# Kernel tuning notes

Hardware: AMD Instinct MI355X
Metric: run time of the kernel (lower is better)

The kernel has to match this reference:

```python
import jax, jax.numpy as jnp
import numpy as np

N_NODES = 100000
HIDDEN = 128
N_EDGES = 640000


def setup_inputs() -> dict:
    key = jax.random.key(0)
    ks = jax.random.split(key, 7)
    x = jax.random.normal(ks[0], (N_NODES, HIDDEN), dtype=jnp.float32)
    # torch Linear weights, stored transposed for y = h @ W + b
    W1 = jax.random.normal(ks[1], (HIDDEN, HIDDEN), dtype=jnp.float32) * (1.0 / np.sqrt(HIDDEN))
    b1 = jax.random.normal(ks[2], (HIDDEN,), dtype=jnp.float32) * 0.01
    W2 = jax.random.normal(ks[3], (HIDDEN, 1), dtype=jnp.float32) * (1.0 / np.sqrt(HIDDEN))
    b2 = jax.random.normal(ks[4], (1,), dtype=jnp.float32) * 0.01
    edge_index = jax.random.randint(ks[5], (2, N_EDGES), 0, N_NODES, dtype=jnp.int64 if jax.config.jax_enable_x64 else jnp.int32)
    edge_index_neg = jax.random.randint(ks[6], (2, N_EDGES), 0, N_NODES, dtype=jnp.int64 if jax.config.jax_enable_x64 else jnp.int32)
    return {"x": x, "W1": W1, "b1": b1, "W2": W2, "b2": b2,
            "edge_index": edge_index, "edge_index_neg": edge_index_neg}


def _decode(x, W1, b1, W2, b2, ei):
    # gather endpoints and Hadamard product: [E, hidden]
    h = x[ei[0]] * x[ei[1]]
    # decoder = ReLU -> Linear(h,h) -> ReLU -> Linear(h,1); then sigmoid
    h = jax.nn.relu(h)
    h = jax.nn.relu(h @ W1 + b1)
    return jax.nn.sigmoid(h @ W2 + b2)  # [E, 1]


def reference(x, W1, b1, W2, b2, edge_index, edge_index_neg):
    edge_pos_pred = _decode(x, W1, b1, W2, b2, edge_index)
    edge_neg_pred = _decode(x, W1, b1, W2, b2, edge_index_neg)
    return jnp.concatenate([edge_pos_pred, edge_neg_pred], axis=0)  # [2E, 1]
```

## Files before the change

### kernel.cpp

```cpp
#include <hip/hip_runtime.h>
#include <hip/hip_bf16.h>

#define HID   128
#define PITCH 136
#define TPB   256

typedef __attribute__((ext_vector_type(8))) __bf16 bf16x8;
typedef __attribute__((ext_vector_type(4))) __bf16 bf16x4;
typedef __attribute__((ext_vector_type(4))) float  f32x4;

__global__ __launch_bounds__(TPB) void prep_kernel(
    const float* __restrict__ W1, __bf16* __restrict__ w1t,
    const float* __restrict__ x, __bf16* __restrict__ xb, int n_x4) {
  if (xb) {
    for (int i = blockIdx.x * TPB + threadIdx.x; i < n_x4; i += gridDim.x * TPB) {
      float4 a = reinterpret_cast<const float4*>(x)[i];
      bf16x4 v;
      v[0] = (__bf16)a.x; v[1] = (__bf16)a.y; v[2] = (__bf16)a.z; v[3] = (__bf16)a.w;
      reinterpret_cast<bf16x4*>(xb)[i] = v;
    }
  }
  if (blockIdx.x == 0 && w1t) {
    __shared__ float w[HID * HID];
    for (int i = threadIdx.x; i < HID * HID; i += TPB) w[i] = W1[i];
    __syncthreads();
    for (int c = threadIdx.x; c < HID * (HID / 8); c += TPB) {
      int n  = c >> 4;
      int k0 = (c & 15) << 3;
      bf16x8 v;
#pragma unroll
      for (int j = 0; j < 8; ++j) v[j] = (__bf16)w[(k0 + j) * HID + n];
      *reinterpret_cast<bf16x8*>(&w1t[n * PITCH + k0]) = v;
    }
  }
}

__global__ __launch_bounds__(TPB) void vgae_decode_kernel(
    const __bf16* __restrict__ xb,
    const __bf16* __restrict__ w1t,
    const float* __restrict__ b1,
    const float* __restrict__ W2,
    const float* __restrict__ b2,
    const int* __restrict__ eip,
    const int* __restrict__ ein,
    float* __restrict__ out,
    int E, int n_tiles)
{
  __shared__ __bf16 sW[HID * PITCH];
  __shared__ float  sb1[HID];
  __shared__ float  sw2[HID];

  {
    const uint4* srcp = reinterpret_cast<const uint4*>(w1t);
    uint4*       dstp = reinterpret_cast<uint4*>(sW);
    for (int i = threadIdx.x; i < (HID * PITCH) / 8; i += TPB) dstp[i] = srcp[i];
  }
  if (threadIdx.x < HID) {
    sb1[threadIdx.x] = b1[threadIdx.x];
    sw2[threadIdx.x] = W2[threadIdx.x];
  }
  __syncthreads();

  const int lane = threadIdx.x & 63;
  const int wave = threadIdx.x >> 6;
  const int m    = lane & 15;
  const int quad = lane >> 4;
  const float b2v = b2[0];

  int tile = blockIdx.x;
  int nsrc = 0, ndst = 0;
  if (tile < n_tiles) {
    const int e_base = tile * 64 + wave * 16;
    const int* ei = (e_base < E) ? eip : ein;
    const int  eo = (e_base < E) ? e_base : (e_base - E);
    nsrc = ei[eo + m];
    ndst = ei[E + eo + m];
  }

  for (; tile < n_tiles; tile += gridDim.x) {
    const int src = nsrc, dst = ndst;
    const __bf16* xs = xb + (size_t)src * HID;
    const __bf16* xd = xb + (size_t)dst * HID;

    bf16x8 S[4], D[4];
#pragma unroll
    for (int kt = 0; kt < 4; ++kt) {
      const int k0 = kt * 32 + quad * 8;
      S[kt] = *reinterpret_cast<const bf16x8*>(xs + k0);
      D[kt] = *reinterpret_cast<const bf16x8*>(xd + k0);
    }

    const int tn = tile + gridDim.x;
    if (tn < n_tiles) {
      const int e_base = tn * 64 + wave * 16;
      const int* ei = (e_base < E) ? eip : ein;
      const int  eo = (e_base < E) ? e_base : (e_base - E);
      nsrc = ei[eo + m];
      ndst = ei[E + eo + m];
    }

    f32x4 acc[8] = {};

#pragma unroll
    for (int kt = 0; kt < 4; ++kt) {
      const int k0 = kt * 32 + quad * 8;
      bf16x8 a;
#pragma unroll
      for (int j = 0; j < 8; ++j) {
        float p = (float)S[kt][j] * (float)D[kt][j];
        a[j] = (__bf16)fmaxf(p, 0.f);
      }
#pragma unroll
      for (int nt = 0; nt < 8; ++nt) {
        bf16x8 bfr = *reinterpret_cast<const bf16x8*>(&sW[(nt * 16 + m) * PITCH + k0]);
        acc[nt] = __builtin_amdgcn_mfma_f32_16x16x32_bf16(a, bfr, acc[nt], 0, 0, 0);
      }
    }

    float p[4] = {0.f, 0.f, 0.f, 0.f};
#pragma unroll
    for (int nt = 0; nt < 8; ++nt) {
      const int n = nt * 16 + m;
      const float b1n = sb1[n];
      const float w2n = sw2[n];
#pragma unroll
      for (int r = 0; r < 4; ++r) {
        float t = fmaxf(acc[nt][r] + b1n, 0.f);
        p[r] = fmaf(t, w2n, p[r]);
      }
    }
#pragma unroll
    for (int off = 1; off < 16; off <<= 1) {
#pragma unroll
      for (int r = 0; r < 4; ++r) p[r] += __shfl_xor(p[r], off, 64);
    }
    if (m == 0) {
      float4 o;
      o.x = 1.f / (1.f + __expf(-(p[0] + b2v)));
      o.y = 1.f / (1.f + __expf(-(p[1] + b2v)));
      o.z = 1.f / (1.f + __expf(-(p[2] + b2v)));
      o.w = 1.f / (1.f + __expf(-(p[3] + b2v)));
      *reinterpret_cast<float4*>(out + tile * 64 + wave * 16 + quad * 4) = o;
    }
  }
}

__global__ __launch_bounds__(TPB) void vgae_decode_fallback(
    const float* __restrict__ x,
    const float* __restrict__ W1,
    const float* __restrict__ b1,
    const float* __restrict__ W2,
    const float* __restrict__ b2,
    const int* __restrict__ eip,
    const int* __restrict__ ein,
    float* __restrict__ out,
    int E, int n_tiles)
{
  __shared__ __bf16 sW[HID * PITCH];
  __shared__ float  sb1[HID];
  __shared__ float  sw2[HID];
  for (int c = threadIdx.x; c < HID * (HID / 8); c += TPB) {
    int n = c >> 4, k0 = (c & 15) << 3;
    bf16x8 v;
#pragma unroll
    for (int j = 0; j < 8; ++j) v[j] = (__bf16)W1[(k0 + j) * HID + n];
    *reinterpret_cast<bf16x8*>(&sW[n * PITCH + k0]) = v;
  }
  if (threadIdx.x < HID) { sb1[threadIdx.x] = b1[threadIdx.x]; sw2[threadIdx.x] = W2[threadIdx.x]; }
  __syncthreads();
  const int lane = threadIdx.x & 63, wave = threadIdx.x >> 6;
  const int m = lane & 15, quad = lane >> 4;
  const float b2v = b2[0];
  for (int tile = blockIdx.x; tile < n_tiles; tile += gridDim.x) {
    const int e_base = tile * 64 + wave * 16;
    const int* ei = (e_base < E) ? eip : ein;
    const int  eo = (e_base < E) ? e_base : (e_base - E);
    const int src = ei[eo + m], dst = ei[E + eo + m];
    const float* xs = x + (size_t)src * HID;
    const float* xd = x + (size_t)dst * HID;
    f32x4 acc[8] = {};
#pragma unroll
    for (int kt = 0; kt < 4; ++kt) {
      const int k0 = kt * 32 + quad * 8;
      float4 s0 = *reinterpret_cast<const float4*>(xs + k0);
      float4 s1 = *reinterpret_cast<const float4*>(xs + k0 + 4);
      float4 d0 = *reinterpret_cast<const float4*>(xd + k0);
      float4 d1 = *reinterpret_cast<const float4*>(xd + k0 + 4);
      bf16x8 a;
      a[0] = (__bf16)fmaxf(s0.x * d0.x, 0.f); a[1] = (__bf16)fmaxf(s0.y * d0.y, 0.f);
      a[2] = (__bf16)fmaxf(s0.z * d0.z, 0.f); a[3] = (__bf16)fmaxf(s0.w * d0.w, 0.f);
      a[4] = (__bf16)fmaxf(s1.x * d1.x, 0.f); a[5] = (__bf16)fmaxf(s1.y * d1.y, 0.f);
      a[6] = (__bf16)fmaxf(s1.z * d1.z, 0.f); a[7] = (__bf16)fmaxf(s1.w * d1.w, 0.f);
#pragma unroll
      for (int nt = 0; nt < 8; ++nt) {
        bf16x8 bfr = *reinterpret_cast<const bf16x8*>(&sW[(nt * 16 + m) * PITCH + k0]);
        acc[nt] = __builtin_amdgcn_mfma_f32_16x16x32_bf16(a, bfr, acc[nt], 0, 0, 0);
      }
    }
    float p[4] = {0.f, 0.f, 0.f, 0.f};
#pragma unroll
    for (int nt = 0; nt < 8; ++nt) {
      const int n = nt * 16 + m;
      const float b1n = sb1[n], w2n = sw2[n];
#pragma unroll
      for (int r = 0; r < 4; ++r) p[r] = fmaf(fmaxf(acc[nt][r] + b1n, 0.f), w2n, p[r]);
    }
#pragma unroll
    for (int off = 1; off < 16; off <<= 1)
#pragma unroll
      for (int r = 0; r < 4; ++r) p[r] += __shfl_xor(p[r], off, 64);
    if (m == 0) {
      float4 o;
      o.x = 1.f / (1.f + __expf(-(p[0] + b2v)));
      o.y = 1.f / (1.f + __expf(-(p[1] + b2v)));
      o.z = 1.f / (1.f + __expf(-(p[2] + b2v)));
      o.w = 1.f / (1.f + __expf(-(p[3] + b2v)));
      *reinterpret_cast<float4*>(out + tile * 64 + wave * 16 + quad * 4) = o;
    }
  }
}

extern "C" void kernel_launch(void* const* d_in, const int* in_sizes, int n_in,
                              void* d_out, int out_size, void* d_ws, size_t ws_size,
                              hipStream_t stream) {
  const float* x  = (const float*)d_in[0];
  const float* W1 = (const float*)d_in[1];
  const float* b1 = (const float*)d_in[2];
  const float* W2 = (const float*)d_in[3];
  const float* b2 = (const float*)d_in[4];
  const int*  eip = (const int*)d_in[5];
  const int*  ein = (const int*)d_in[6];
  float* out = (float*)d_out;
  const int E = in_sizes[5] / 2;
  const int n_tiles = (2 * E) / 64;
  const int n_nodes = in_sizes[0] / HID;
  const int n_x4 = in_sizes[0] / 4;

  const size_t w1t_bytes = (size_t)HID * PITCH * sizeof(__bf16);
  const size_t xb_off    = 65536;
  const size_t xb_bytes  = (size_t)n_nodes * HID * sizeof(__bf16);

  __bf16* w1t = nullptr;
  __bf16* xb  = nullptr;
  if (ws_size >= w1t_bytes) w1t = (__bf16*)d_ws;
  if (ws_size >= xb_off + xb_bytes) xb = (__bf16*)((char*)d_ws + xb_off);

  if (w1t && xb) {
    int prep_grid = (n_x4 + TPB - 1) / TPB;
    if (prep_grid > 6400) prep_grid = 6400;
    prep_kernel<<<prep_grid, TPB, 0, stream>>>(W1, w1t, x, xb, n_x4);
    vgae_decode_kernel<<<2560, TPB, 0, stream>>>(xb, w1t, b1, W2, b2,
                                                 eip, ein, out, E, n_tiles);
  } else {
    vgae_decode_fallback<<<2560, TPB, 0, stream>>>(x, W1, b1, W2, b2,
                                                   eip, ein, out, E, n_tiles);
  }
}
```

Before: 224.7 us.

## Software-pipeline node feature gathers one tile ahead of MFMA compute

Restructures the persistent tile loop so the bf16 feature rows for the next tile are gathered while the current tile's Hadamard/ReLU operands are already in registers, and edge indices are prefetched two tiles ahead. This aims to hide gather latency behind the MFMA matmul. The grid is also changed to 2500 blocks and capped at n_tiles, which balances tiles per block. Costs are extra live registers (S, D, a[4]), which may lower occupancy.

```diff
diff --git a/kernel.cpp b/kernel.cpp
--- a/kernel.cpp
+++ b/kernel.cpp
@@ -68,52 +68,72 @@
   const float b2v = b2[0];
 
   int tile = blockIdx.x;
+  bf16x8 S[4], D[4];
   int nsrc = 0, ndst = 0;
+
   if (tile < n_tiles) {
     const int e_base = tile * 64 + wave * 16;
     const int* ei = (e_base < E) ? eip : ein;
     const int  eo = (e_base < E) ? e_base : (e_base - E);
-    nsrc = ei[eo + m];
-    ndst = ei[E + eo + m];
-  }
-
-  for (; tile < n_tiles; tile += gridDim.x) {
-    const int src = nsrc, dst = ndst;
+    const int src = ei[eo + m];
+    const int dst = ei[E + eo + m];
     const __bf16* xs = xb + (size_t)src * HID;
     const __bf16* xd = xb + (size_t)dst * HID;
-
-    bf16x8 S[4], D[4];
 #pragma unroll
     for (int kt = 0; kt < 4; ++kt) {
       const int k0 = kt * 32 + quad * 8;
       S[kt] = *reinterpret_cast<const bf16x8*>(xs + k0);
       D[kt] = *reinterpret_cast<const bf16x8*>(xd + k0);
     }
-
     const int tn = tile + gridDim.x;
     if (tn < n_tiles) {
-      const int e_base = tn * 64 + wave * 16;
-      const int* ei = (e_base < E) ? eip : ein;
-      const int  eo = (e_base < E) ? e_base : (e_base - E);
-      nsrc = ei[eo + m];
-      ndst = ei[E + eo + m];
-    }
-
-    f32x4 acc[8] = {};
-
-#pragma unroll
-    for (int kt = 0; kt < 4; ++kt) {
-      const int k0 = kt * 32 + quad * 8;
-      bf16x8 a;
+      const int e2 = tn * 64 + wave * 16;
+      const int* ei2 = (e2 < E) ? eip : ein;
+      const int  eo2 = (e2 < E) ? e2 : (e2 - E);
+      nsrc = ei2[eo2 + m];
+      ndst = ei2[E + eo2 + m];
+    }
+  }
+
+  for (; tile < n_tiles; tile += gridDim.x) {
+    bf16x8 a[4];
+#pragma unroll
+    for (int kt = 0; kt < 4; ++kt) {
 #pragma unroll
       for (int j = 0; j < 8; ++j) {
         float p = (float)S[kt][j] * (float)D[kt][j];
-        a[j] = (__bf16)fmaxf(p, 0.f);
-      }
+        a[kt][j] = (__bf16)fmaxf(p, 0.f);
+      }
+    }
+
+    const int tn = tile + gridDim.x;
+    if (tn < n_tiles) {
+      const __bf16* xs = xb + (size_t)nsrc * HID;
+      const __bf16* xd = xb + (size_t)ndst * HID;
+#pragma unroll
+      for (int kt = 0; kt < 4; ++kt) {
+        const int k0 = kt * 32 + quad * 8;
+        S[kt] = *reinterpret_cast<const bf16x8*>(xs + k0);
+        D[kt] = *reinterpret_cast<const bf16x8*>(xd + k0);
+      }
+      const int tnn = tn + gridDim.x;
+      if (tnn < n_tiles) {
+        const int e2 = tnn * 64 + wave * 16;
+        const int* ei2 = (e2 < E) ? eip : ein;
+        const int  eo2 = (e2 < E) ? e2 : (e2 - E);
+        nsrc = ei2[eo2 + m];
+        ndst = ei2[E + eo2 + m];
+      }
+    }
+
+    f32x4 acc[8] = {};
+#pragma unroll
+    for (int kt = 0; kt < 4; ++kt) {
+      const int k0 = kt * 32 + quad * 8;
 #pragma unroll
       for (int nt = 0; nt < 8; ++nt) {
         bf16x8 bfr = *reinterpret_cast<const bf16x8*>(&sW[(nt * 16 + m) * PITCH + k0]);
-        acc[nt] = __builtin_amdgcn_mfma_f32_16x16x32_bf16(a, bfr, acc[nt], 0, 0, 0);
+        acc[nt] = __builtin_amdgcn_mfma_f32_16x16x32_bf16(a[kt], bfr, acc[nt], 0, 0, 0);
       }
     }
 
@@ -249,7 +269,9 @@
     int prep_grid = (n_x4 + TPB - 1) / TPB;
     if (prep_grid > 6400) prep_grid = 6400;
     prep_kernel<<<prep_grid, TPB, 0, stream>>>(W1, w1t, x, xb, n_x4);
-    vgae_decode_kernel<<<2560, TPB, 0, stream>>>(xb, w1t, b1, W2, b2,
+    int grid = 2500;
+    if (grid > n_tiles) grid = n_tiles;
+    vgae_decode_kernel<<<grid, TPB, 0, stream>>>(xb, w1t, b1, W2, b2,
                                                  eip, ein, out, E, n_tiles);
   } else {
     vgae_decode_fallback<<<2560, TPB, 0, stream>>>(x, W1, b1, W2, b2,
```

Measured after the change: 269.9 us. 1.2x slower.

## Process two edge tiles per iteration to overlap gathers with MFMA compute

Applied to the files above, without the earlier changes.

The decode loop now handles pairs of 64-edge tiles. The second tile's gathered node rows are loaded while the first tile's MFMA and epilogue run, and indices for the next pair are prefetched. The aim is to hide gather latency behind matrix work within a single wave. In exchange, register pressure rises, and launch_bounds(256,4) plus a grid of 2500 are added to keep occupancy. An even tile count is now required to take this path; otherwise the fallback kernel runs.

```diff
diff --git a/kernel.cpp b/kernel.cpp
--- a/kernel.cpp
+++ b/kernel.cpp
@@ -35,7 +35,7 @@
   }
 }
 
-__global__ __launch_bounds__(TPB) void vgae_decode_kernel(
+__global__ __launch_bounds__(TPB, 4) void vgae_decode_kernel(
     const __bf16* __restrict__ xb,
     const __bf16* __restrict__ w1t,
     const float* __restrict__ b1,
@@ -66,81 +66,139 @@
   const int m    = lane & 15;
   const int quad = lane >> 4;
   const float b2v = b2[0];
-
-  int tile = blockIdx.x;
-  int nsrc = 0, ndst = 0;
-  if (tile < n_tiles) {
-    const int e_base = tile * 64 + wave * 16;
-    const int* ei = (e_base < E) ? eip : ein;
-    const int  eo = (e_base < E) ? e_base : (e_base - E);
-    nsrc = ei[eo + m];
-    ndst = ei[E + eo + m];
-  }
-
-  for (; tile < n_tiles; tile += gridDim.x) {
-    const int src = nsrc, dst = ndst;
-    const __bf16* xs = xb + (size_t)src * HID;
-    const __bf16* xd = xb + (size_t)dst * HID;
+  const int n_pairs = n_tiles >> 1;
+
+  int pair = blockIdx.x;
+  int sA = 0, dA = 0, sB = 0, dB = 0;
+  if (pair < n_pairs) {
+    const int eb = pair * 128 + wave * 16;
+    const int* eiA = (eb < E) ? eip : ein;
+    const int  eoA = (eb < E) ? eb : (eb - E);
+    sA = eiA[eoA + m];           dA = eiA[E + eoA + m];
+    const int eb2 = eb + 64;
+    const int* eiB = (eb2 < E) ? eip : ein;
+    const int  eoB = (eb2 < E) ? eb2 : (eb2 - E);
+    sB = eiB[eoB + m];           dB = eiB[E + eoB + m];
+  }
+
+  for (; pair < n_pairs; pair += gridDim.x) {
+    const int tileA = 2 * pair;
+    const __bf16* xsA = xb + (size_t)sA * HID;
+    const __bf16* xdA = xb + (size_t)dA * HID;
+    const __bf16* xsB = xb + (size_t)sB * HID;
+    const __bf16* xdB = xb + (size_t)dB * HID;
 
     bf16x8 S[4], D[4];
 #pragma unroll
     for (int kt = 0; kt < 4; ++kt) {
       const int k0 = kt * 32 + quad * 8;
-      S[kt] = *reinterpret_cast<const bf16x8*>(xs + k0);
-      D[kt] = *reinterpret_cast<const bf16x8*>(xd + k0);
-    }
-
-    const int tn = tile + gridDim.x;
-    if (tn < n_tiles) {
-      const int e_base = tn * 64 + wave * 16;
-      const int* ei = (e_base < E) ? eip : ein;
-      const int  eo = (e_base < E) ? e_base : (e_base - E);
-      nsrc = ei[eo + m];
-      ndst = ei[E + eo + m];
-    }
-
-    f32x4 acc[8] = {};
-
-#pragma unroll
-    for (int kt = 0; kt < 4; ++kt) {
-      const int k0 = kt * 32 + quad * 8;
-      bf16x8 a;
+      S[kt] = *reinterpret_cast<const bf16x8*>(xsA + k0);
+      D[kt] = *reinterpret_cast<const bf16x8*>(xdA + k0);
+    }
+
+    const int np = pair + gridDim.x;
+    if (np < n_pairs) {
+      const int eb = np * 128 + wave * 16;
+      const int* eiA = (eb < E) ? eip : ein;
+      const int  eoA = (eb < E) ? eb : (eb - E);
+      sA = eiA[eoA + m];           dA = eiA[E + eoA + m];
+      const int eb2 = eb + 64;
+      const int* eiB = (eb2 < E) ? eip : ein;
+      const int  eoB = (eb2 < E) ? eb2 : (eb2 - E);
+      sB = eiB[eoB + m];           dB = eiB[E + eoB + m];
+    }
+
+    bf16x8 aA[4];
+#pragma unroll
+    for (int kt = 0; kt < 4; ++kt) {
 #pragma unroll
       for (int j = 0; j < 8; ++j) {
         float p = (float)S[kt][j] * (float)D[kt][j];
-        a[j] = (__bf16)fmaxf(p, 0.f);
-      }
+        aA[kt][j] = (__bf16)fmaxf(p, 0.f);
+      }
+    }
+
+#pragma unroll
+    for (int kt = 0; kt < 4; ++kt) {
+      const int k0 = kt * 32 + quad * 8;
+      S[kt] = *reinterpret_cast<const bf16x8*>(xsB + k0);
+      D[kt] = *reinterpret_cast<const bf16x8*>(xdB + k0);
+    }
+
+    {
+      f32x4 acc[8] = {};
+#pragma unroll
+      for (int kt = 0; kt < 4; ++kt) {
+        const int k0 = kt * 32 + quad * 8;
+#pragma unroll
+        for (int nt = 0; nt < 8; ++nt) {
+          bf16x8 bfr = *reinterpret_cast<const bf16x8*>(&sW[(nt * 16 + m) * PITCH + k0]);
+          acc[nt] = __builtin_amdgcn_mfma_f32_16x16x32_bf16(aA[kt], bfr, acc[nt], 0, 0, 0);
+        }
+      }
+      float p[4] = {0.f, 0.f, 0.f, 0.f};
 #pragma unroll
       for (int nt = 0; nt < 8; ++nt) {
-        bf16x8 bfr = *reinterpret_cast<const bf16x8*>(&sW[(nt * 16 + m) * PITCH + k0]);
-        acc[nt] = __builtin_amdgcn_mfma_f32_16x16x32_bf16(a, bfr, acc[nt], 0, 0, 0);
-      }
-    }
-
-    float p[4] = {0.f, 0.f, 0.f, 0.f};
-#pragma unroll
-    for (int nt = 0; nt < 8; ++nt) {
-      const int n = nt * 16 + m;
-      const float b1n = sb1[n];
-      const float w2n = sw2[n];
-#pragma unroll
-      for (int r = 0; r < 4; ++r) {
-        float t = fmaxf(acc[nt][r] + b1n, 0.f);
-        p[r] = fmaf(t, w2n, p[r]);
-      }
-    }
-#pragma unroll
-    for (int off = 1; off < 16; off <<= 1) {
-#pragma unroll
-      for (int r = 0; r < 4; ++r) p[r] += __shfl_xor(p[r], off, 64);
-    }
-    if (m == 0) {
-      float4 o;
-      o.x = 1.f / (1.f + __expf(-(p[0] + b2v)));
-      o.y = 1.f / (1.f + __expf(-(p[1] + b2v)));
-      o.z = 1.f / (1.f + __expf(-(p[2] + b2v)));
-      o.w = 1.f / (1.f + __expf(-(p[3] + b2v)));
-      *reinterpret_cast<float4*>(out + tile * 64 + wave * 16 + quad * 4) = o;
+        const int n = nt * 16 + m;
+        const float b1n = sb1[n], w2n = sw2[n];
+#pragma unroll
+        for (int r = 0; r < 4; ++r) p[r] = fmaf(fmaxf(acc[nt][r] + b1n, 0.f), w2n, p[r]);
+      }
+#pragma unroll
+      for (int off = 1; off < 16; off <<= 1)
+#pragma unroll
+        for (int r = 0; r < 4; ++r) p[r] += __shfl_xor(p[r], off, 64);
+      if (m == 0) {
+        float4 o;
+        o.x = 1.f / (1.f + __expf(-(p[0] + b2v)));
+        o.y = 1.f / (1.f + __expf(-(p[1] + b2v)));
+        o.z = 1.f / (1.f + __expf(-(p[2] + b2v)));
+        o.w = 1.f / (1.f + __expf(-(p[3] + b2v)));
+        *reinterpret_cast<float4*>(out + tileA * 64 + wave * 16 + quad * 4) = o;
+      }
+    }
+
+    bf16x8 aB[4];
+#pragma unroll
+    for (int kt = 0; kt < 4; ++kt) {
+#pragma unroll
+      for (int j = 0; j < 8; ++j) {
+        float p = (float)S[kt][j] * (float)D[kt][j];
+        aB[kt][j] = (__bf16)fmaxf(p, 0.f);
+      }
+    }
+
+    {
+      f32x4 acc[8] = {};
+#pragma unroll
+      for (int kt = 0; kt < 4; ++kt) {
+        const int k0 = kt * 32 + quad * 8;
+#pragma unroll
+        for (int nt = 0; nt < 8; ++nt) {
+          bf16x8 bfr = *reinterpret_cast<const bf16x8*>(&sW[(nt * 16 + m) * PITCH + k0]);
+          acc[nt] = __builtin_amdgcn_mfma_f32_16x16x32_bf16(aB[kt], bfr, acc[nt], 0, 0, 0);
+        }
+      }
+      float p[4] = {0.f, 0.f, 0.f, 0.f};
+#pragma unroll
+      for (int nt = 0; nt < 8; ++nt) {
+        const int n = nt * 16 + m;
+        const float b1n = sb1[n], w2n = sw2[n];
+#pragma unroll
+        for (int r = 0; r < 4; ++r) p[r] = fmaf(fmaxf(acc[nt][r] + b1n, 0.f), w2n, p[r]);
+      }
+#pragma unroll
+      for (int off = 1; off < 16; off <<= 1)
+#pragma unroll
+        for (int r = 0; r < 4; ++r) p[r] += __shfl_xor(p[r], off, 64);
+      if (m == 0) {
+        float4 o;
+        o.x = 1.f / (1.f + __expf(-(p[0] + b2v)));
+        o.y = 1.f / (1.f + __expf(-(p[1] + b2v)));
+        o.z = 1.f / (1.f + __expf(-(p[2] + b2v)));
+        o.w = 1.f / (1.f + __expf(-(p[3] + b2v)));
+        *reinterpret_cast<float4*>(out + (tileA + 1) * 64 + wave * 16 + quad * 4) = o;
+      }
     }
   }
 }
@@ -245,11 +303,14 @@
   if (ws_size >= w1t_bytes) w1t = (__bf16*)d_ws;
   if (ws_size >= xb_off + xb_bytes) xb = (__bf16*)((char*)d_ws + xb_off);
 
-  if (w1t && xb) {
+  if (w1t && xb && (n_tiles % 2 == 0)) {
     int prep_grid = (n_x4 + TPB - 1) / TPB;
     if (prep_grid > 6400) prep_grid = 6400;
     prep_kernel<<<prep_grid, TPB, 0, stream>>>(W1, w1t, x, xb, n_x4);
-    vgae_decode_kernel<<<2560, TPB, 0, stream>>>(xb, w1t, b1, W2, b2,
+    int n_pairs = n_tiles / 2;
+    int grid = 2500;
+    if (grid > n_pairs) grid = n_pairs;
+    vgae_decode_kernel<<<grid, TPB, 0, stream>>>(xb, w1t, b1, W2, b2,
                                                  eip, ein, out, E, n_tiles);
   } else {
     vgae_decode_fallback<<<2560, TPB, 0, stream>>>(x, W1, b1, W2, b2,
```

Measured after the change: 501.6 us. 123% more time.
